# Optimization experiments

Hardware: AMD Instinct MI355X
Metric: run time of the kernel (lower is better)

## Reference

```python
import jax, jax.numpy as jnp
import numpy as np

B, S, D, H, HID = 2, 2048, 256, 8, 1024
EPS = 1e-9


def gelu_fast(x):
    return 0.5 * x * (1.0 + jnp.tanh(x * 0.7978845608 * (1.0 + 0.044715 * x * x)))


def layer_norm(x, g, b):
    m = jnp.mean(x, axis=-1, keepdims=True)
    v = jnp.mean(jnp.square(x - m), axis=-1, keepdims=True)
    return (x - m) * jax.lax.rsqrt(v + EPS) * g + b


def setup_inputs() -> dict:
    key = jax.random.key(0)
    ks = jax.random.split(key, 16)
    x = jax.random.normal(ks[0], (B, S, D), dtype=jnp.float32)
    # causal look-ahead mask: additive, 0 on/below diagonal, -1e9 above
    causal = jnp.triu(jnp.ones((S, S), dtype=jnp.float32), k=1) * (-1e9)
    look_ahead_mask = causal[None, None, :, :]  # (1,1,S,S)
    sd = 0.02
    return {
        "x": x,
        "look_ahead_mask": look_ahead_mask,
        "ln1_g": jnp.ones((D,), jnp.float32),
        "ln1_b": jnp.zeros((D,), jnp.float32),
        "wq_w": jax.random.normal(ks[1], (D * H, D), jnp.float32) * sd,
        "wq_b": jnp.zeros((D * H,), jnp.float32),
        "wk_w": jax.random.normal(ks[2], (D * H, D), jnp.float32) * sd,
        "wk_b": jnp.zeros((D * H,), jnp.float32),
        "wv_w": jax.random.normal(ks[3], (D * H, D), jnp.float32) * sd,
        "wv_b": jnp.zeros((D * H,), jnp.float32),
        "dense_w": jax.random.normal(ks[4], (D, D * H), jnp.float32) * sd,
        "dense_b": jnp.zeros((D,), jnp.float32),
        "ln2_g": jnp.ones((D,), jnp.float32),
        "ln2_b": jnp.zeros((D,), jnp.float32),
        "fc1_w": jax.random.normal(ks[5], (HID, D), jnp.float32) * sd,
        "fc1_b": jnp.zeros((HID,), jnp.float32),
        "fc2_w": jax.random.normal(ks[6], (D, HID), jnp.float32) * sd,
        "fc2_b": jnp.zeros((D,), jnp.float32),
    }


def reference(x, look_ahead_mask, ln1_g, ln1_b, wq_w, wq_b, wk_w, wk_b,
              wv_w, wv_b, dense_w, dense_b, ln2_g, ln2_b,
              fc1_w, fc1_b, fc2_w, fc2_b):
    xn = layer_norm(x, ln1_g, ln1_b)
    # QKV: D -> D*H, each head has full head-dim D (module quirk)
    q = (jnp.einsum('bsd,ed->bse', xn, wq_w) + wq_b).reshape(B, S, H, D).transpose(0, 2, 1, 3)
    k = (jnp.einsum('bsd,ed->bse', xn, wk_w) + wk_b).reshape(B, S, H, D).transpose(0, 2, 1, 3)
    v = (jnp.einsum('bsd,ed->bse', xn, wv_w) + wv_b).reshape(B, S, H, D).transpose(0, 2, 1, 3)
    scores = jnp.einsum('bhqd,bhkd->bhqk', q, k) / jnp.sqrt(jnp.float32(D))
    scores = scores + look_ahead_mask
    attn_weights = jax.nn.softmax(scores, axis=-1)
    ctx = jnp.einsum('bhqk,bhkd->bhqd', attn_weights, v)  # (B,H,S,D)
    ctx = ctx.transpose(0, 2, 1, 3).reshape(B, S, H * D)
    attn = jnp.einsum('bse,de->bsd', ctx, dense_w) + dense_b
    x1 = xn + attn  # residual uses post-LN x (module quirk)
    m = layer_norm(x1, ln2_g, ln2_b)
    m = gelu_fast(jnp.einsum('bsd,hd->bsh', m, fc1_w) + fc1_b)
    m = jnp.einsum('bsh,dh->bsd', m, fc2_w) + fc2_b
    out = x1 + m
    return out, attn_weights
```

## Files before the change

kernel.cpp:

```cpp
#include <hip/hip_runtime.h>
#include <hip/hip_bf16.h>


typedef __bf16 bf16_t;
typedef __bf16 bf16x8 __attribute__((ext_vector_type(8)));
typedef __bf16 bf16x4 __attribute__((ext_vector_type(4)));
typedef float  f32x4  __attribute__((ext_vector_type(4)));

#define DEV __device__ __forceinline__

DEV f32x4 mfma16(bf16x8 a, bf16x8 b, f32x4 c) {
  return __builtin_amdgcn_mfma_f32_16x16x32_bf16(a, b, c, 0, 0, 0);
}

DEV void gload16(const void* g, void* l) {
  __builtin_amdgcn_global_load_lds(
      (const __attribute__((address_space(1))) unsigned int*)g,
      (__attribute__((address_space(3))) unsigned int*)l, 16, 0, 0);
}

__global__ __launch_bounds__(256) void k1_lncvt(
    const float* __restrict__ x, const float* __restrict__ g, const float* __restrict__ bta,
    float* __restrict__ of, bf16_t* __restrict__ ob,
    const float* __restrict__ s0, const float* __restrict__ s1,
    const float* __restrict__ s2, const float* __restrict__ s3,
    const float* __restrict__ s4, const float* __restrict__ s5,
    bf16_t* __restrict__ d0, bf16_t* __restrict__ d1, bf16_t* __restrict__ d2,
    bf16_t* __restrict__ d3, bf16_t* __restrict__ d4, bf16_t* __restrict__ d5) {
  int bid = blockIdx.x;
  if (bid < 1024) {
    int row = bid * 4 + (threadIdx.x >> 6);
    int l = threadIdx.x & 63;
    const float4 v = *(const float4*)(x + (size_t)row * 256 + l * 4);
    float s  = v.x + v.y + v.z + v.w;
    float s2 = v.x*v.x + v.y*v.y + v.z*v.z + v.w*v.w;
#pragma unroll
    for (int o = 1; o < 64; o <<= 1) { s += __shfl_xor(s, o, 64); s2 += __shfl_xor(s2, o, 64); }
    float m   = s * (1.f/256.f);
    float var = s2 * (1.f/256.f) - m * m;
    float rs  = rsqrtf(var + 1e-9f);
    const float4 gv = *(const float4*)(g   + l * 4);
    const float4 bv = *(const float4*)(bta + l * 4);
    float4 y;
    y.x = (v.x - m) * rs * gv.x + bv.x;
    y.y = (v.y - m) * rs * gv.y + bv.y;
    y.z = (v.z - m) * rs * gv.z + bv.z;
    y.w = (v.w - m) * rs * gv.w + bv.w;
    *(float4*)(of + (size_t)row * 256 + l * 4) = y;
    bf16x4 yb = { (bf16_t)y.x, (bf16_t)y.y, (bf16_t)y.z, (bf16_t)y.w };
    *(bf16x4*)(ob + (size_t)row * 256 + l * 4) = yb;
  } else {
    int i = (bid - 1024) * 256 + threadIdx.x;
    const float* s; bf16_t* d; int off;
    if      (i < 131072) { s = s0; d = d0; off = i; }
    else if (i < 262144) { s = s1; d = d1; off = i - 131072; }
    else if (i < 393216) { s = s2; d = d2; off = i - 262144; }
    else if (i < 524288) { s = s3; d = d3; off = i - 393216; }
    else if (i < 589824) { s = s4; d = d4; off = i - 524288; }
    else                 { s = s5; d = d5; off = i - 589824; }
    float4 v = ((const float4*)s)[off];
    bf16x4 o = { (bf16_t)v.x, (bf16_t)v.y, (bf16_t)v.z, (bf16_t)v.w };
    ((bf16x4*)d)[off] = o;
  }
}

DEV void gemm_core(const bf16_t* __restrict__ A, const bf16_t* __restrict__ W,
                   int lda, int row0, int col0, int k0, int kiters,
                   char* Asb, char* Bsb, f32x4 (&acc)[4][4]) {
  int tid = threadIdx.x, w = tid >> 6, l = tid & 63, l15 = l & 15, lhi = l >> 4;
  int wr = (w >> 1) * 64, wc = (w & 1) * 64;

#define STAGE(buf, kk) do {                                                   \
    char* Ad = Asb + (buf) * 8192 + w * 1024;                                 \
    char* Bd = Bsb + (buf) * 8192 + w * 1024;                                 \
    _Pragma("unroll")                                                         \
    for (int j = 0; j < 2; ++j) {                                             \
      int idx = (j * 256 + tid) * 8; int r = idx >> 5, c = idx & 31;          \
      gload16(A + (size_t)(row0 + r) * lda + (kk) + c, Ad + j * 4096);        \
      gload16(W + (size_t)(col0 + r) * lda + (kk) + c, Bd + j * 4096);        \
    } } while (0)

  STAGE(0, k0);
  for (int t = 0; t < kiters; ++t) {
    int cur = t & 1;
    if (t + 1 < kiters) {
      STAGE(cur ^ 1, k0 + (t + 1) * 32);
      asm volatile("s_waitcnt vmcnt(4)" ::: "memory");
    } else {
      asm volatile("s_waitcnt vmcnt(0)" ::: "memory");
    }
    __builtin_amdgcn_s_barrier();
    asm volatile("" ::: "memory");
    const bf16_t* As = (const bf16_t*)(Asb + cur * 8192);
    const bf16_t* Bs = (const bf16_t*)(Bsb + cur * 8192);
    bf16x8 af[4], bfr[4];
#pragma unroll
    for (int m = 0; m < 4; ++m)
      af[m] = *(const bf16x8*)(As + (wr + 16 * m + l15) * 32 + lhi * 8);
#pragma unroll
    for (int n = 0; n < 4; ++n)
      bfr[n] = *(const bf16x8*)(Bs + (wc + 16 * n + l15) * 32 + lhi * 8);
#pragma unroll
    for (int m = 0; m < 4; ++m)
#pragma unroll
      for (int n = 0; n < 4; ++n)
        acc[m][n] = mfma16(af[m], bfr[n], acc[m][n]);
    asm volatile("s_waitcnt lgkmcnt(0)" ::: "memory");
    __builtin_amdgcn_s_barrier();
  }
#undef STAGE
}

__global__ __launch_bounds__(256, 4) void gemm_qkv(
    const bf16_t* __restrict__ A,
    const bf16_t* __restrict__ W0, const bf16_t* __restrict__ W1, const bf16_t* __restrict__ W2,
    const float* __restrict__ b0, const float* __restrict__ b1, const float* __restrict__ b2,
    bf16_t* __restrict__ qo, bf16_t* __restrict__ ko, bf16_t* __restrict__ vto) {
  __shared__ char smem[34816];
  char* Asb = smem;
  char* Bsb = smem + 16384;
  int bx = blockIdx.x;
  int wsel = bx >> 4, cb = bx & 15;
  const bf16_t* W    = wsel == 0 ? W0 : (wsel == 1 ? W1 : W2);
  const float*  bias = wsel == 0 ? b0 : (wsel == 1 ? b1 : b2);
  int row0 = blockIdx.y * 128, col0 = cb * 128;
  f32x4 acc[4][4] = {};
  gemm_core(A, W, 256, row0, col0, 0, 8, Asb, Bsb, acc);

  int tid = threadIdx.x, w = tid >> 6, l = tid & 63, l15 = l & 15, lhi = l >> 4;
  int wr = (w >> 1) * 64, wc = (w & 1) * 64;

  if (wsel < 2) {
    bf16_t* out = wsel == 0 ? qo : ko;
#pragma unroll
    for (int m = 0; m < 4; ++m)
#pragma unroll
      for (int n = 0; n < 4; ++n)
#pragma unroll
        for (int j = 0; j < 4; ++j) {
          int row = row0 + wr + 16 * m + lhi * 4 + j;
          int col = col0 + wc + 16 * n + l15;
          float v = acc[m][n][j] + bias[col];
          out[((size_t)((row >> 11) * 8 + (col >> 8)) * 2048 + (row & 2047)) * 256 + (col & 255)] = (bf16_t)v;
        }
  } else {
    __syncthreads();
    bf16_t* T = (bf16_t*)smem;
#pragma unroll
    for (int m = 0; m < 4; ++m)
#pragma unroll
      for (int n = 0; n < 4; ++n) {
        int d = wc + 16 * n + l15;
        int s = wr + 16 * m + lhi * 4;
        bf16x4 v4;
#pragma unroll
        for (int j = 0; j < 4; ++j) v4[j] = (bf16_t)(acc[m][n][j] + bias[col0 + d]);
        *(bf16x4*)(T + d * 136 + s) = v4;
      }
    __syncthreads();
    int bh = ((row0 >> 11) << 3) + (col0 >> 8);
    int d0 = col0 & 255, s0g = row0 & 2047;
#pragma unroll
    for (int p = 0; p < 8; ++p) {
      int idx = p * 256 + tid;
      int d = idx >> 4, c = (idx & 15) * 8;
      bf16x8 v8 = *(const bf16x8*)(T + d * 136 + c);
      *(bf16x8*)(vto + ((size_t)bh * 256 + d0 + d) * 2048 + s0g + c) = v8;
    }
  }
}

__global__ __launch_bounds__(256, 4) void gemm_part(
    const bf16_t* __restrict__ A, const bf16_t* __restrict__ W,
    int lda, int ksub, float* __restrict__ parts) {
  __shared__ char Asb[2 * 8192];
  __shared__ char Bsb[2 * 8192];
  int z = blockIdx.z;
  int row0 = blockIdx.y * 128, col0 = blockIdx.x * 128;
  f32x4 acc[4][4] = {};
  gemm_core(A, W, lda, row0, col0, z * ksub, ksub >> 5, Asb, Bsb, acc);

  int tid = threadIdx.x, w = tid >> 6, l = tid & 63, l15 = l & 15, lhi = l >> 4;
  int wr = (w >> 1) * 64, wc = (w & 1) * 64;
  float* p = parts + (size_t)z * 1048576;
#pragma unroll
  for (int m = 0; m < 4; ++m)
#pragma unroll
    for (int n = 0; n < 4; ++n)
#pragma unroll
      for (int j = 0; j < 4; ++j) {
        int row = row0 + wr + 16 * m + lhi * 4 + j;
        int col = col0 + wc + 16 * n + l15;
        p[(size_t)row * 256 + col] = acc[m][n][j];
      }
}

__global__ __launch_bounds__(256) void reduce4(
    const float* __restrict__ parts, const float* __restrict__ bias,
    const float* __restrict__ res, float* __restrict__ out) {
  int i = blockIdx.x * 256 + threadIdx.x;
  f32x4 s = *(const f32x4*)(parts + (size_t)i * 4);
  s += *(const f32x4*)(parts + 1048576 + (size_t)i * 4);
  s += *(const f32x4*)(parts + 2097152 + (size_t)i * 4);
  s += *(const f32x4*)(parts + 3145728 + (size_t)i * 4);
  s += *(const f32x4*)(res + (size_t)i * 4);
  s += *(const f32x4*)(bias + (i & 63) * 4);
  *(f32x4*)(out + (size_t)i * 4) = s;
}

__global__ __launch_bounds__(256) void reduce_ln(
    const float* __restrict__ parts, const float* __restrict__ bias,
    const float* __restrict__ res, const float* __restrict__ g,
    const float* __restrict__ bta, float* __restrict__ x1o, bf16_t* __restrict__ mo) {
  int row = blockIdx.x * 4 + (threadIdx.x >> 6);
  int l = threadIdx.x & 63;
  size_t base = (size_t)row * 256 + l * 4;
  f32x4 s = *(const f32x4*)(parts + base);
  s += *(const f32x4*)(parts + 1048576 + base);
  s += *(const f32x4*)(parts + 2097152 + base);
  s += *(const f32x4*)(parts + 3145728 + base);
  s += *(const f32x4*)(res + base);
  s += *(const f32x4*)(bias + l * 4);
  *(f32x4*)(x1o + base) = s;
  float sm = s[0] + s[1] + s[2] + s[3];
  float s2 = s[0]*s[0] + s[1]*s[1] + s[2]*s[2] + s[3]*s[3];
#pragma unroll
  for (int o = 1; o < 64; o <<= 1) { sm += __shfl_xor(sm, o, 64); s2 += __shfl_xor(s2, o, 64); }
  float m   = sm * (1.f/256.f);
  float var = s2 * (1.f/256.f) - m * m;
  float rs  = rsqrtf(var + 1e-9f);
  const float4 gv = *(const float4*)(g   + l * 4);
  const float4 bv = *(const float4*)(bta + l * 4);
  bf16x4 yb;
  yb[0] = (bf16_t)((s[0] - m) * rs * gv.x + bv.x);
  yb[1] = (bf16_t)((s[1] - m) * rs * gv.y + bv.y);
  yb[2] = (bf16_t)((s[2] - m) * rs * gv.z + bv.z);
  yb[3] = (bf16_t)((s[3] - m) * rs * gv.w + bv.w);
  *(bf16x4*)(mo + base) = yb;
}

__global__ __launch_bounds__(256, 4) void gemm_fc1(
    const bf16_t* __restrict__ A, const bf16_t* __restrict__ W,
    const float* __restrict__ bias, bf16_t* __restrict__ out) {
  __shared__ char Asb[2 * 8192];
  __shared__ char Bsb[2 * 8192];
  int row0 = blockIdx.y * 128, col0 = blockIdx.x * 128;
  f32x4 acc[4][4] = {};
  gemm_core(A, W, 256, row0, col0, 0, 8, Asb, Bsb, acc);

  int tid = threadIdx.x, w = tid >> 6, l = tid & 63, l15 = l & 15, lhi = l >> 4;
  int wr = (w >> 1) * 64, wc = (w & 1) * 64;
#pragma unroll
  for (int m = 0; m < 4; ++m)
#pragma unroll
    for (int n = 0; n < 4; ++n)
#pragma unroll
      for (int j = 0; j < 4; ++j) {
        int row = row0 + wr + 16 * m + lhi * 4 + j;
        int col = col0 + wc + 16 * n + l15;
        float t = acc[m][n][j] + bias[col];
        float ge = 0.5f * t * (1.f + tanhf(0.7978845608f * t * (1.f + 0.044715f * t * t)));
        out[(size_t)row * 1024 + col] = (bf16_t)ge;
      }
}

__global__ __launch_bounds__(256, 2) void attn_fused(
    const bf16_t* __restrict__ qg, const bf16_t* __restrict__ kg,
    const bf16_t* __restrict__ vt, float* __restrict__ pout,
    bf16_t* __restrict__ ctxo) {
  __shared__ __align__(16) char smem[74368];
  char*  Ksh   = smem;
  char*  Psh   = smem + 65536;
  float* sl    = (float*)(smem + 73728);
  float* invsh = (float*)(smem + 74240);
  int bx = blockIdx.x;
  int bh = bx & 15, qt = 63 - (bx >> 4);
  int tid = threadIdx.x, w = tid >> 6, l = tid & 63;
  int l15 = l & 15, lhi = l >> 4;
  const bf16_t* Q = qg + (size_t)bh * 2048 * 256;
  const bf16_t* K = kg + (size_t)bh * 2048 * 256;
  const bf16_t* V = vt + (size_t)bh * 256 * 2048;
  int qbase = qt * 32;
  int nkt = (qt >> 1) + 1;

  bf16x8 qf[2][8];
#pragma unroll
  for (int m = 0; m < 2; ++m)
#pragma unroll
    for (int ks = 0; ks < 8; ++ks)
      qf[m][ks] = *(const bf16x8*)(Q + (size_t)(qbase + m * 16 + l15) * 256 + ks * 32 + lhi * 8);

#define KSTAGE(td_, ts_) do {                                                  \
    char* dst0 = Ksh + ((td_) & 1) * 32768 + w * 1024;                         \
    _Pragma("unroll")                                                          \
    for (int j5 = 0; j5 < 8; ++j5) {                                           \
      int idx = j5 * 4096 + tid * 16; int r = idx >> 9; int inner = idx & 511; \
      int colb = inner ^ ((r & 15) << 4);                                      \
      gload16(K + (size_t)((ts_) * 64 + r) * 256 + (colb >> 1), dst0 + j5 * 4096); \
    } } while (0)

  int krow = w * 16 + l15;
  int ksw  = (krow & 15) << 4;

  KSTAGE(0, 0);
  asm volatile("s_waitcnt vmcnt(0)" ::: "memory");
  __builtin_amdgcn_s_barrier();

  float sums[2][4] = {};
  for (int t = 0; t < nkt; ++t) {
    int tn = (t + 1 < nkt) ? t + 1 : nkt - 1;
    KSTAGE(t + 1, tn);
    const char* Kb = Ksh + (t & 1) * 32768;
    f32x4 acc[2] = {};
    __builtin_amdgcn_s_setprio(1);
#pragma unroll
    for (int ks = 0; ks < 8; ++ks) {
      bf16x8 kb = *(const bf16x8*)(Kb + krow * 512 + ((ks * 64 + lhi * 16) ^ ksw));
      acc[0] = mfma16(qf[0][ks], kb, acc[0]);
      acc[1] = mfma16(qf[1][ks], kb, acc[1]);
    }
    __builtin_amdgcn_s_setprio(0);
#pragma unroll
    for (int m = 0; m < 2; ++m)
#pragma unroll
      for (int j = 0; j < 4; ++j) {
        int qr = qbase + m * 16 + lhi * 4 + j;
        int kc = t * 64 + krow;
        sums[m][j] += (kc <= qr) ? __expf(acc[m][j] * 0.0625f) : 0.f;
      }
    asm volatile("s_waitcnt vmcnt(0)" ::: "memory");
    __builtin_amdgcn_s_barrier();
  }

#pragma unroll
  for (int m = 0; m < 2; ++m)
#pragma unroll
    for (int j = 0; j < 4; ++j)
#pragma unroll
      for (int o = 1; o < 16; o <<= 1)
        sums[m][j] += __shfl_xor(sums[m][j], o, 64);
  if (l15 == 0)
#pragma unroll
    for (int m = 0; m < 2; ++m)
#pragma unroll
      for (int j = 0; j < 4; ++j)
        sl[w * 32 + m * 16 + lhi * 4 + j] = sums[m][j];
  __syncthreads();
  if (tid < 32)
    invsh[tid] = 1.f / (sl[tid] + sl[32 + tid] + sl[64 + tid] + sl[96 + tid]);
  __syncthreads();
  float inv4[2][4];
#pragma unroll
  for (int m = 0; m < 2; ++m)
#pragma unroll
    for (int j = 0; j < 4; ++j)
      inv4[m][j] = invsh[m * 16 + lhi * 4 + j];

  KSTAGE(0, 0);
  asm volatile("s_waitcnt vmcnt(0)" ::: "memory");
  __builtin_amdgcn_s_barrier();

  f32x4 ctx[2][4] = {};
  for (int t = 0; t < nkt; ++t) {
    int tn = (t + 1 < nkt) ? t + 1 : nkt - 1;
    KSTAGE(t + 1, tn);
    bf16x8 vb[4][2];
#pragma unroll
    for (int n4 = 0; n4 < 4; ++n4)
#pragma unroll
      for (int ks2 = 0; ks2 < 2; ++ks2)
        vb[n4][ks2] = *(const bf16x8*)(V + (size_t)(w * 64 + n4 * 16 + l15) * 2048 + t * 64 + ks2 * 32 + lhi * 8);

    const char* Kb = Ksh + (t & 1) * 32768;
    f32x4 acc[2] = {};
    __builtin_amdgcn_s_setprio(1);
#pragma unroll
    for (int ks = 0; ks < 8; ++ks) {
      bf16x8 kb = *(const bf16x8*)(Kb + krow * 512 + ((ks * 64 + lhi * 16) ^ ksw));
      acc[0] = mfma16(qf[0][ks], kb, acc[0]);
      acc[1] = mfma16(qf[1][ks], kb, acc[1]);
    }
    __builtin_amdgcn_s_setprio(0);

    char* Pb = Psh + (t & 1) * 4096;
#pragma unroll
    for (int m = 0; m < 2; ++m)
#pragma unroll
      for (int j = 0; j < 4; ++j) {
        int rr = m * 16 + lhi * 4 + j;
        int qr = qbase + rr;
        int kc = t * 64 + krow;
        float e = (kc <= qr) ? __expf(acc[m][j] * 0.0625f) * inv4[m][j] : 0.f;
        pout[((size_t)bh * 2048 + qr) * 2048 + kc] = e;
        *(bf16_t*)(Pb + rr * 128 + ((krow * 2) ^ (lhi << 5))) = (bf16_t)e;
      }
    asm volatile("s_waitcnt lgkmcnt(0)" ::: "memory");
    asm volatile("s_waitcnt vmcnt(16)" ::: "memory");
    __builtin_amdgcn_s_barrier();

    __builtin_amdgcn_s_setprio(1);
#pragma unroll
    for (int ks2 = 0; ks2 < 2; ++ks2) {
      bf16x8 pa[2];
#pragma unroll
      for (int m = 0; m < 2; ++m) {
        int pr = m * 16 + l15;
        pa[m] = *(const bf16x8*)(Pb + pr * 128 + ((ks2 * 64 + lhi * 16) ^ (((pr >> 2) & 3) << 5)));
      }
#pragma unroll
      for (int m = 0; m < 2; ++m)
#pragma unroll
        for (int n4 = 0; n4 < 4; ++n4)
          ctx[m][n4] = mfma16(pa[m], vb[n4][ks2], ctx[m][n4]);
    }
    __builtin_amdgcn_s_setprio(0);
  }
#undef KSTAGE

  int b = bh >> 3, h = bh & 7;
#pragma unroll
  for (int m = 0; m < 2; ++m)
#pragma unroll
    for (int n4 = 0; n4 < 4; ++n4)
#pragma unroll
      for (int j = 0; j < 4; ++j) {
        int qr = qbase + m * 16 + lhi * 4 + j;
        ctxo[((size_t)b * 2048 + qr) * 2048 + h * 256 + w * 64 + n4 * 16 + l15] = (bf16_t)ctx[m][n4][j];
      }

  int zs = nkt * 64;
  for (int r = 0; r < 32; ++r) {
    size_t base2 = ((size_t)bh * 2048 + qbase + r) * 2048;
    for (int c = zs + tid * 4; c < 2048; c += 1024)
      *(float4*)(pout + base2 + c) = make_float4(0.f, 0.f, 0.f, 0.f);
  }
}

extern "C" void kernel_launch(void* const* d_in, const int* in_sizes, int n_in,
                              void* d_out, int out_size, void* d_ws, size_t ws_size,
                              hipStream_t stream) {
  const float* x     = (const float*)d_in[0];
  const float* ln1g  = (const float*)d_in[2];
  const float* ln1b  = (const float*)d_in[3];
  const float* wq_w  = (const float*)d_in[4];
  const float* wq_b  = (const float*)d_in[5];
  const float* wk_w  = (const float*)d_in[6];
  const float* wk_b  = (const float*)d_in[7];
  const float* wv_w  = (const float*)d_in[8];
  const float* wv_b  = (const float*)d_in[9];
  const float* dw    = (const float*)d_in[10];
  const float* db    = (const float*)d_in[11];
  const float* ln2g  = (const float*)d_in[12];
  const float* ln2b  = (const float*)d_in[13];
  const float* f1w   = (const float*)d_in[14];
  const float* f1b   = (const float*)d_in[15];
  const float* f2w   = (const float*)d_in[16];
  const float* f2b   = (const float*)d_in[17];

  char* ws = (char*)d_ws;
  const size_t MB = 1u << 20;
  float*  xn_f = (float*) (ws + 0 * MB);
  bf16_t* xn_b = (bf16_t*)(ws + 4 * MB);
  bf16_t* q_b  = (bf16_t*)(ws + 6 * MB);
  bf16_t* k_b  = (bf16_t*)(ws + 22 * MB);
  bf16_t* ctx_b= (bf16_t*)(ws + 38 * MB);
  bf16_t* vt_b = (bf16_t*)(ws + 54 * MB);
  float*  x1_f = (float*) (ws + 70 * MB);
  bf16_t* m_b  = (bf16_t*)(ws + 74 * MB);
  bf16_t* h_b  = (bf16_t*)(ws + 76 * MB);
  bf16_t* wq_bf = (bf16_t*)(ws + 84 * MB);
  bf16_t* wk_bf = wq_bf + 524288;
  bf16_t* wv_bf = wk_bf + 524288;
  bf16_t* dw_bf = wv_bf + 524288;
  bf16_t* f1_bf = dw_bf + 524288;
  bf16_t* f2_bf = f1_bf + 262144;
  float* parts_d = (float*)q_b;
  float* parts_f = (float*)k_b;

  float* out0 = (float*)d_out;
  float* pout = out0 + 1048576;

  k1_lncvt<<<3584, 256, 0, stream>>>(x, ln1g, ln1b, xn_f, xn_b,
                                     wq_w, wk_w, wv_w, dw, f1w, f2w,
                                     wq_bf, wk_bf, wv_bf, dw_bf, f1_bf, f2_bf);

  gemm_qkv<<<dim3(48, 32), 256, 0, stream>>>(xn_b, wq_bf, wk_bf, wv_bf,
                                             wq_b, wk_b, wv_b, q_b, k_b, vt_b);

  attn_fused<<<1024, 256, 0, stream>>>(q_b, k_b, vt_b, pout, ctx_b);

  gemm_part<<<dim3(2, 32, 4), 256, 0, stream>>>(ctx_b, dw_bf, 2048, 512, parts_d);
  reduce_ln<<<1024, 256, 0, stream>>>(parts_d, db, xn_f, ln2g, ln2b, x1_f, m_b);

  gemm_fc1<<<dim3(8, 32), 256, 0, stream>>>(m_b, f1_bf, f1b, h_b);

  gemm_part<<<dim3(2, 32, 4), 256, 0, stream>>>(h_b, f2_bf, 1024, 256, parts_f);
  reduce4<<<1024, 256, 0, stream>>>(parts_f, f2b, x1_f, out0);
}
```

Measured before the change: 231.9 us.

## Shrink attention K tile to 32 keys and raise occupancy to four blocks

The fused attention kernel now stages 32-key K tiles instead of 64, and splits the four waves 2x2 over query rows and key columns, so each wave holds one Q fragment set. Shared memory drops to about 40 KB and launch bounds ask for four blocks per CU. Blocks are remapped in a serpentine order over query tiles for better load balance, and causal skipping becomes finer, so less masked work is done. The cost is twice as many loop iterations and barriers per block, with less MFMA work between each sync.

```diff
diff --git a/kernel.cpp b/kernel.cpp
--- a/kernel.cpp
+++ b/kernel.cpp
@@ -264,155 +264,143 @@
       }
 }
 
-__global__ __launch_bounds__(256, 2) void attn_fused(
+__global__ __launch_bounds__(256, 4) void attn_fused(
     const bf16_t* __restrict__ qg, const bf16_t* __restrict__ kg,
     const bf16_t* __restrict__ vt, float* __restrict__ pout,
     bf16_t* __restrict__ ctxo) {
-  __shared__ __align__(16) char smem[74368];
-  char*  Ksh   = smem;
-  char*  Psh   = smem + 65536;
-  float* sl    = (float*)(smem + 73728);
-  float* invsh = (float*)(smem + 74240);
+  __shared__ __align__(16) char smem[40960];
+  char* Ksh = smem;
+  char* Psh = smem + 32768;
+  float* sl    = (float*)(smem + 32768);
+  float* invsh = sl + 64;
+
   int bx = blockIdx.x;
-  int bh = bx & 15, qt = 63 - (bx >> 4);
+  int bh = bx & 15;
+  int r4 = bx >> 8, g4 = (bx >> 4) & 15;
+  int tq = 16 * r4 + ((r4 & 1) ? (15 - g4) : g4);
+  int qt = 63 - tq;
+  int qbase = qt * 32;
+  int nkt = qt + 1;
+
   int tid = threadIdx.x, w = tid >> 6, l = tid & 63;
   int l15 = l & 15, lhi = l >> 4;
+  int wm = w >> 1, wn = w & 1;
   const bf16_t* Q = qg + (size_t)bh * 2048 * 256;
   const bf16_t* K = kg + (size_t)bh * 2048 * 256;
   const bf16_t* V = vt + (size_t)bh * 256 * 2048;
-  int qbase = qt * 32;
-  int nkt = (qt >> 1) + 1;
-
-  bf16x8 qf[2][8];
-#pragma unroll
-  for (int m = 0; m < 2; ++m)
-#pragma unroll
-    for (int ks = 0; ks < 8; ++ks)
-      qf[m][ks] = *(const bf16x8*)(Q + (size_t)(qbase + m * 16 + l15) * 256 + ks * 32 + lhi * 8);
+
+  bf16x8 qf[8];
+#pragma unroll
+  for (int ks = 0; ks < 8; ++ks)
+    qf[ks] = *(const bf16x8*)(Q + (size_t)(qbase + wm * 16 + l15) * 256 + ks * 32 + lhi * 8);
 
 #define KSTAGE(td_, ts_) do {                                                  \
-    char* dst0 = Ksh + ((td_) & 1) * 32768 + w * 1024;                         \
+    char* dst0 = Ksh + ((td_) & 1) * 16384 + w * 4096;                         \
     _Pragma("unroll")                                                          \
-    for (int j5 = 0; j5 < 8; ++j5) {                                           \
-      int idx = j5 * 4096 + tid * 16; int r = idx >> 9; int inner = idx & 511; \
-      int colb = inner ^ ((r & 15) << 4);                                      \
-      gload16(K + (size_t)((ts_) * 64 + r) * 256 + (colb >> 1), dst0 + j5 * 4096); \
+    for (int j5 = 0; j5 < 4; ++j5) {                                           \
+      int idxb = w * 4096 + j5 * 1024 + (tid & 63) * 16;                       \
+      int rr5 = idxb >> 9; int inner = idxb & 511;                             \
+      int colb = inner ^ ((rr5 & 15) << 4);                                    \
+      gload16(K + (size_t)((ts_) * 32 + rr5) * 256 + (colb >> 1), dst0 + j5 * 1024); \
     } } while (0)
 
-  int krow = w * 16 + l15;
+  int krow = wn * 16 + l15;
   int ksw  = (krow & 15) << 4;
 
   KSTAGE(0, 0);
   asm volatile("s_waitcnt vmcnt(0)" ::: "memory");
   __builtin_amdgcn_s_barrier();
 
-  float sums[2][4] = {};
+  float sums[4] = {};
   for (int t = 0; t < nkt; ++t) {
     int tn = (t + 1 < nkt) ? t + 1 : nkt - 1;
     KSTAGE(t + 1, tn);
-    const char* Kb = Ksh + (t & 1) * 32768;
-    f32x4 acc[2] = {};
+    const char* Kb = Ksh + (t & 1) * 16384;
+    f32x4 acc = {};
     __builtin_amdgcn_s_setprio(1);
 #pragma unroll
     for (int ks = 0; ks < 8; ++ks) {
       bf16x8 kb = *(const bf16x8*)(Kb + krow * 512 + ((ks * 64 + lhi * 16) ^ ksw));
-      acc[0] = mfma16(qf[0][ks], kb, acc[0]);
-      acc[1] = mfma16(qf[1][ks], kb, acc[1]);
+      acc = mfma16(qf[ks], kb, acc);
     }
     __builtin_amdgcn_s_setprio(0);
 #pragma unroll
-    for (int m = 0; m < 2; ++m)
-#pragma unroll
-      for (int j = 0; j < 4; ++j) {
-        int qr = qbase + m * 16 + lhi * 4 + j;
-        int kc = t * 64 + krow;
-        sums[m][j] += (kc <= qr) ? __expf(acc[m][j] * 0.0625f) : 0.f;
-      }
+    for (int j = 0; j < 4; ++j) {
+      int qr = qbase + wm * 16 + lhi * 4 + j;
+      int kc = t * 32 + krow;
+      sums[j] += (kc <= qr) ? __expf(acc[j] * 0.0625f) : 0.f;
+    }
     asm volatile("s_waitcnt vmcnt(0)" ::: "memory");
     __builtin_amdgcn_s_barrier();
   }
 
 #pragma unroll
-  for (int m = 0; m < 2; ++m)
+  for (int j = 0; j < 4; ++j)
+#pragma unroll
+    for (int o = 1; o < 16; o <<= 1)
+      sums[j] += __shfl_xor(sums[j], o, 64);
+  if (l15 == 0)
 #pragma unroll
     for (int j = 0; j < 4; ++j)
-#pragma unroll
-      for (int o = 1; o < 16; o <<= 1)
-        sums[m][j] += __shfl_xor(sums[m][j], o, 64);
-  if (l15 == 0)
-#pragma unroll
-    for (int m = 0; m < 2; ++m)
-#pragma unroll
-      for (int j = 0; j < 4; ++j)
-        sl[w * 32 + m * 16 + lhi * 4 + j] = sums[m][j];
+      sl[wn * 32 + wm * 16 + lhi * 4 + j] = sums[j];
   __syncthreads();
-  if (tid < 32)
-    invsh[tid] = 1.f / (sl[tid] + sl[32 + tid] + sl[64 + tid] + sl[96 + tid]);
+  if (tid < 32) invsh[tid] = 1.f / (sl[tid] + sl[32 + tid]);
   __syncthreads();
-  float inv4[2][4];
-#pragma unroll
-  for (int m = 0; m < 2; ++m)
-#pragma unroll
-    for (int j = 0; j < 4; ++j)
-      inv4[m][j] = invsh[m * 16 + lhi * 4 + j];
+  float inv4[4];
+#pragma unroll
+  for (int j = 0; j < 4; ++j)
+    inv4[j] = invsh[wm * 16 + lhi * 4 + j];
 
   KSTAGE(0, 0);
   asm volatile("s_waitcnt vmcnt(0)" ::: "memory");
+  asm volatile("s_waitcnt lgkmcnt(0)" ::: "memory");
   __builtin_amdgcn_s_barrier();
 
   f32x4 ctx[2][4] = {};
   for (int t = 0; t < nkt; ++t) {
     int tn = (t + 1 < nkt) ? t + 1 : nkt - 1;
     KSTAGE(t + 1, tn);
-    bf16x8 vb[4][2];
+    bf16x8 vb[4];
 #pragma unroll
     for (int n4 = 0; n4 < 4; ++n4)
-#pragma unroll
-      for (int ks2 = 0; ks2 < 2; ++ks2)
-        vb[n4][ks2] = *(const bf16x8*)(V + (size_t)(w * 64 + n4 * 16 + l15) * 2048 + t * 64 + ks2 * 32 + lhi * 8);
-
-    const char* Kb = Ksh + (t & 1) * 32768;
-    f32x4 acc[2] = {};
+      vb[n4] = *(const bf16x8*)(V + (size_t)(w * 64 + n4 * 16 + l15) * 2048 + t * 32 + lhi * 8);
+
+    const char* Kb = Ksh + (t & 1) * 16384;
+    f32x4 acc = {};
     __builtin_amdgcn_s_setprio(1);
 #pragma unroll
     for (int ks = 0; ks < 8; ++ks) {
       bf16x8 kb = *(const bf16x8*)(Kb + krow * 512 + ((ks * 64 + lhi * 16) ^ ksw));
-      acc[0] = mfma16(qf[0][ks], kb, acc[0]);
-      acc[1] = mfma16(qf[1][ks], kb, acc[1]);
+      acc = mfma16(qf[ks], kb, acc);
     }
     __builtin_amdgcn_s_setprio(0);
 
     char* Pb = Psh + (t & 1) * 4096;
 #pragma unroll
+    for (int j = 0; j < 4; ++j) {
+      int rr = wm * 16 + lhi * 4 + j;
+      int qr = qbase + rr;
+      int kc = t * 32 + krow;
+      float e = (kc <= qr) ? __expf(acc[j] * 0.0625f) * inv4[j] : 0.f;
+      pout[((size_t)bh * 2048 + qr) * 2048 + kc] = e;
+      *(bf16_t*)(Pb + ((rr * 64 + krow * 2) ^ ((rr & 3) << 4))) = (bf16_t)e;
+    }
+    asm volatile("s_waitcnt lgkmcnt(0)" ::: "memory");
+    asm volatile("s_waitcnt vmcnt(8)" ::: "memory");
+    __builtin_amdgcn_s_barrier();
+
+    bf16x8 pa[2];
+#pragma unroll
+    for (int m = 0; m < 2; ++m) {
+      int pr = m * 16 + l15;
+      pa[m] = *(const bf16x8*)(Pb + ((pr * 64 + lhi * 16) ^ ((pr & 3) << 4)));
+    }
+    __builtin_amdgcn_s_setprio(1);
+#pragma unroll
     for (int m = 0; m < 2; ++m)
 #pragma unroll
-      for (int j = 0; j < 4; ++j) {
-        int rr = m * 16 + lhi * 4 + j;
-        int qr = qbase + rr;
-        int kc = t * 64 + krow;
-        float e = (kc <= qr) ? __expf(acc[m][j] * 0.0625f) * inv4[m][j] : 0.f;
-        pout[((size_t)bh * 2048 + qr) * 2048 + kc] = e;
-        *(bf16_t*)(Pb + rr * 128 + ((krow * 2) ^ (lhi << 5))) = (bf16_t)e;
-      }
-    asm volatile("s_waitcnt lgkmcnt(0)" ::: "memory");
-    asm volatile("s_waitcnt vmcnt(16)" ::: "memory");
-    __builtin_amdgcn_s_barrier();
-
-    __builtin_amdgcn_s_setprio(1);
-#pragma unroll
-    for (int ks2 = 0; ks2 < 2; ++ks2) {
-      bf16x8 pa[2];
-#pragma unroll
-      for (int m = 0; m < 2; ++m) {
-        int pr = m * 16 + l15;
-        pa[m] = *(const bf16x8*)(Pb + pr * 128 + ((ks2 * 64 + lhi * 16) ^ (((pr >> 2) & 3) << 5)));
-      }
-#pragma unroll
-      for (int m = 0; m < 2; ++m)
-#pragma unroll
-        for (int n4 = 0; n4 < 4; ++n4)
-          ctx[m][n4] = mfma16(pa[m], vb[n4][ks2], ctx[m][n4]);
-    }
+      for (int n4 = 0; n4 < 4; ++n4)
+        ctx[m][n4] = mfma16(pa[m], vb[n4], ctx[m][n4]);
     __builtin_amdgcn_s_setprio(0);
   }
 #undef KSTAGE
@@ -428,7 +416,7 @@
         ctxo[((size_t)b * 2048 + qr) * 2048 + h * 256 + w * 64 + n4 * 16 + l15] = (bf16_t)ctx[m][n4][j];
       }
 
-  int zs = nkt * 64;
+  int zs = qbase + 32;
   for (int r = 0; r < 32; ++r) {
     size_t base2 = ((size_t)bh * 2048 + qbase + r) * 2048;
     for (int c = zs + tid * 4; c < 2048; c += 1024)
```

After: 318.3 us. +37.2%, slower.
